# Kernel optimization log

Measured on AMD Instinct MI355X. Metric: run time of the kernel, lower is better.

## Reference

```python
import jax, jax.numpy as jnp
import numpy as np

# dims
B, T, H = 4, 2048, 768
HEADS, D = 4, 768          # GATConv(out_channels=768, heads=4, concat=False)
L = 3                      # num_layers
WIN = 2
K = 2 * WIN + 1
EPS = 1e-5
NEG_SLOPE = 0.2            # PyG GATConv leaky_relu slope


def setup_inputs() -> dict:
    key = jax.random.key(0)
    ks = jax.random.split(key, 4)
    s = 1.0 / np.sqrt(H)
    x = jax.random.normal(ks[0], (B, T, H), jnp.float32)
    W = jax.random.normal(ks[1], (L, H, HEADS, D), jnp.float32) * s   # lin weights per layer
    a_src = jax.random.normal(ks[2], (L, HEADS, D), jnp.float32) * s  # att_src
    a_dst = jax.random.normal(ks[3], (L, HEADS, D), jnp.float32) * s  # att_dst
    bias = jnp.zeros((L, D), jnp.float32)                             # GATConv bias (concat=False -> [D])
    gamma = jnp.ones((L, H), jnp.float32)                             # LayerNorm weight
    beta = jnp.zeros((L, H), jnp.float32)                             # LayerNorm bias
    return {"x": x, "W": W, "a_src": a_src, "a_dst": a_dst,
            "bias": bias, "gamma": gamma, "beta": beta}


def _layernorm(z, g, b):
    m = jnp.mean(z, axis=-1, keepdims=True)
    v = jnp.mean((z - m) ** 2, axis=-1, keepdims=True)
    return (z - m) * jax.lax.rsqrt(v + EPS) * g + b


def _gat_layer(x, Wl, asrc_w, adst_w, bias_l, idx, mask):
    # x: [B,T,H]; banded GAT with neighborhoods idx: [T,K] (clipped), mask: [T,K]
    h = jnp.einsum('bti,ihd->bthd', x, Wl)                 # [B,T,heads,D]
    asrc = jnp.einsum('bthd,hd->bth', h, asrc_w)           # per-source-node score term
    adst = jnp.einsum('bthd,hd->bth', h, adst_w)           # per-target-node score term
    h_nb = h[:, idx]                                       # [B,T,K,heads,D] gathered neighbors j
    score = jax.nn.leaky_relu(asrc[:, idx] + adst[:, :, None, :], NEG_SLOPE)  # [B,T,K,heads]
    score = jnp.where(mask[None, :, :, None], score, -jnp.inf)
    attn = jax.nn.softmax(score, axis=2)                   # softmax over incoming edges per target
    out = jnp.einsum('btkh,btkhd->bthd', attn, h_nb)       # weighted aggregation
    return out.mean(axis=2) + bias_l                       # concat=False -> mean over heads


def reference(x, W, a_src, a_dst, bias, gamma, beta):
    # banded neighborhood indices (window edges both directions + self-loop from PyG default)
    offs = jnp.arange(-WIN, WIN + 1)
    idx = jnp.arange(T)[:, None] + offs[None, :]           # [T,K]
    mask = (idx >= 0) & (idx < T)
    idx = jnp.clip(idx, 0, T - 1)
    for l in range(L):
        res = x
        y = _gat_layer(x, W[l], a_src[l], a_dst[l], bias[l], idx, mask)
        x = _layernorm(y + res, gamma[l], beta[l])         # dropout = identity in eval
    return x
```

## Files before the change

### kernel.cpp

```cpp
#include <hip/hip_runtime.h>
#include <stdint.h>

#define TT 2048
#define BB 4
#define HH 768
#define NHEADS 4
#define DD 768
#define NN 3072
#define LL 3
#define BT 8192
#define KNB 5
#define NBLK 12
#define ATPB 4
#define NROWS 8

typedef __bf16 bf16x8 __attribute__((ext_vector_type(8)));
typedef float f32x4 __attribute__((ext_vector_type(4)));

__device__ __forceinline__ unsigned short f2bf(float f){
  union { float f; unsigned u; } v; v.f = f;
  unsigned u = v.u;
  return (unsigned short)((u + 0x7FFFu + ((u >> 16) & 1u)) >> 16);
}
__device__ __forceinline__ float bf2f(unsigned short h){
  union { unsigned u; float f; } v; v.u = ((unsigned)h) << 16;
  return v.f;
}
__device__ __forceinline__ void gload16(const unsigned short* g, unsigned short* l){
  __builtin_amdgcn_global_load_lds((const __attribute__((address_space(1))) void*)g,
                                   (__attribute__((address_space(3))) void*)l, 16, 0, 0);
}

__global__ void wt_kernel(const float* __restrict__ W, unsigned short* __restrict__ Wt){
  __shared__ float tile[32][33];
  int l = blockIdx.z;
  int n0 = blockIdx.x * 32, k0 = blockIdx.y * 32;
  int tx = threadIdx.x, ty = threadIdx.y;
  const float* Wl = W + (size_t)l * HH * NN;
  for (int r = 0; r < 4; r++)
    tile[ty + r*8][tx] = Wl[(size_t)(k0 + ty + r*8) * NN + n0 + tx];
  __syncthreads();
  unsigned short* Wtl = Wt + (size_t)l * NN * HH;
  for (int r = 0; r < 4; r++){
    int n = n0 + ty + r*8;
    Wtl[(size_t)n * HH + k0 + tx] = f2bf(tile[tx][ty + r*8]);
  }
}

__global__ void xconv_kernel(const float* __restrict__ x, unsigned short* __restrict__ xb){
  int i = blockIdx.x * blockDim.x + threadIdx.x;
  float4 v = ((const float4*)x)[i];
  ushort4 o;
  o.x = f2bf(v.x); o.y = f2bf(v.y); o.z = f2bf(v.z); o.w = f2bf(v.w);
  *(ushort4*)(xb + (size_t)i * 4) = o;
}

#define BM 128
#define BN 128
#define BK 64

__global__ __launch_bounds__(256, 2) void gemm_kernel(
    const unsigned short* __restrict__ xb,
    const unsigned short* __restrict__ wt,
    unsigned short* __restrict__ hout,
    const float* __restrict__ a_srcl,
    const float* __restrict__ a_dstl,
    float* __restrict__ psrc,
    float* __restrict__ pdst){
  __shared__ __align__(16) unsigned short xs[BM][BK];
  __shared__ __align__(16) unsigned short wsd[BN][BK];
  int bm = blockIdx.y * BM;
  int bn = blockIdx.x * BN;
  int tid = threadIdx.x;
  int wave = tid >> 6, lane = tid & 63;
  int m16 = lane & 15, q = lane >> 4;
  int wm = (wave >> 1) * 64, wn = (wave & 1) * 64;
  int r8 = lane >> 3, c8 = lane & 7;
  int cg = (c8 ^ r8) * 8;
  const unsigned short* ga[4]; const unsigned short* gb[4];
  unsigned short* la[4]; unsigned short* lb[4];
  #pragma unroll
  for (int s = 0; s < 4; s++){
    int row = wave * 32 + s * 8;
    ga[s] = xb + (size_t)(bm + row + r8) * HH + cg;
    gb[s] = wt + (size_t)(bn + row + r8) * HH + cg;
    la[s] = &xs[row][0];
    lb[s] = &wsd[row][0];
  }
  int rd0 = ((0 + q) ^ (m16 & 7)) * 8;
  int rd1 = ((4 + q) ^ (m16 & 7)) * 8;
  f32x4 acc[4][4] = {};
  for (int k0 = 0; k0 < HH; k0 += BK){
    #pragma unroll
    for (int s = 0; s < 4; s++){
      gload16(ga[s] + k0, la[s]);
      gload16(gb[s] + k0, lb[s]);
    }
    __syncthreads();
    bf16x8 af[4], bfr[4];
    for (int i = 0; i < 4; i++)
      af[i] = __builtin_bit_cast(bf16x8, *(const uint4*)(&xs[wm + i*16 + m16][rd0]));
    for (int j = 0; j < 4; j++)
      bfr[j] = __builtin_bit_cast(bf16x8, *(const uint4*)(&wsd[wn + j*16 + m16][rd0]));
    for (int i = 0; i < 4; i++)
      for (int j = 0; j < 4; j++)
        acc[i][j] = __builtin_amdgcn_mfma_f32_16x16x32_bf16(af[i], bfr[j], acc[i][j], 0, 0, 0);
    for (int i = 0; i < 4; i++)
      af[i] = __builtin_bit_cast(bf16x8, *(const uint4*)(&xs[wm + i*16 + m16][rd1]));
    for (int j = 0; j < 4; j++)
      bfr[j] = __builtin_bit_cast(bf16x8, *(const uint4*)(&wsd[wn + j*16 + m16][rd1]));
    for (int i = 0; i < 4; i++)
      for (int j = 0; j < 4; j++)
        acc[i][j] = __builtin_amdgcn_mfma_f32_16x16x32_bf16(af[i], bfr[j], acc[i][j], 0, 0, 0);
    __syncthreads();
  }
  for (int i = 0; i < 4; i++){
    int row0 = bm + wm + i*16 + q*4;
    for (int j = 0; j < 4; j++){
      int col = bn + wn + j*16 + m16;
      unsigned short* hp = hout + (size_t)row0 * NN + col;
      hp[0]            = f2bf(acc[i][j][0]);
      hp[NN]           = f2bf(acc[i][j][1]);
      hp[2*(size_t)NN] = f2bf(acc[i][j][2]);
      hp[3*(size_t)NN] = f2bf(acc[i][j][3]);
    }
  }
  int col0 = bn + wn;
  int head = col0 / DD;
  int blk  = (col0 % DD) >> 6;
  float wsrc[4], wdstw[4];
  for (int j = 0; j < 4; j++){
    int n = col0 + j*16 + m16;
    wsrc[j]  = a_srcl[n];
    wdstw[j] = a_dstl[n];
  }
  for (int i = 0; i < 4; i++){
    for (int reg = 0; reg < 4; reg++){
      float ss = 0.f, dd = 0.f;
      for (int j = 0; j < 4; j++){
        float v = acc[i][j][reg];
        ss += v * wsrc[j];
        dd += v * wdstw[j];
      }
      ss += __shfl_xor(ss, 1, 64); dd += __shfl_xor(dd, 1, 64);
      ss += __shfl_xor(ss, 2, 64); dd += __shfl_xor(dd, 2, 64);
      ss += __shfl_xor(ss, 4, 64); dd += __shfl_xor(dd, 4, 64);
      ss += __shfl_xor(ss, 8, 64); dd += __shfl_xor(dd, 8, 64);
      if (m16 == 0){
        int row = bm + wm + i*16 + q*4 + reg;
        size_t slot = (size_t)row * (NHEADS * NBLK) + head * NBLK + blk;
        psrc[slot] = ss;
        pdst[slot] = dd;
      }
    }
  }
}

__global__ __launch_bounds__(384) void attn_ln_kernel(const unsigned short* __restrict__ h,
    const float* __restrict__ psrc, const float* __restrict__ pdst,
    const float* __restrict__ xin_f32,
    const unsigned short* __restrict__ xin_bf,
    const float* __restrict__ bias_l,
    const float* __restrict__ gamma_l, const float* __restrict__ beta_l,
    float* __restrict__ x_out, unsigned short* __restrict__ xb_next,
    int write_f32){
  int bid = blockIdx.x;
  int grp = ((bid & 7) << 8) | (bid >> 3);
  int token0 = grp * ATPB;
  int t0 = token0 & (TT - 1);
  int bseq = token0 >> 11;
  int tid = threadIdx.x;
  int wave = tid >> 6, lane = tid & 63;
  __shared__ __align__(16) unsigned short hs[NROWS][NN];
  __shared__ float attn_s[ATPB][NHEADS][KNB];
  __shared__ float as_sh[NROWS * NHEADS], ad_sh[NROWS * NHEADS];
  __shared__ float part_s[ATPB * 96], part_q[ATPB * 96];
  __shared__ float mv_mean[ATPB], mv_rstd[ATPB];
  #pragma unroll
  for (int j = 0; j < NROWS; j++){
    int g = t0 - 2 + j;
    g = min(max(g, 0), TT - 1);
    const unsigned short* src = h + ((size_t)(bseq * TT + g)) * NN + tid * 8;
    gload16(src, &hs[j][wave * 512]);
  }
  if (tid < 2 * NROWS * NHEADS){
    int which = tid >= NROWS * NHEADS;
    int i = tid & (NROWS * NHEADS - 1);
    int lt = i >> 2, head = i & 3;
    int tcl = min(max(t0 - 2 + lt, 0), TT - 1);
    const float* p = (which ? pdst : psrc) +
        ((size_t)(bseq * TT + tcl) * NHEADS + head) * NBLK;
    float4 a = *(const float4*)(p);
    float4 b = *(const float4*)(p + 4);
    float4 d = *(const float4*)(p + 8);
    float s = a.x+a.y+a.z+a.w + b.x+b.y+b.z+b.w + d.x+d.y+d.z+d.w;
    (which ? ad_sh : as_sh)[i] = s;
  }
  __syncthreads();
  if (tid < ATPB * NHEADS){
    int ti = tid >> 2, head = tid & 3;
    int t = t0 + ti;
    float sc[KNB];
    float mx = -3.0e38f;
    float ad = ad_sh[(ti + 2) * NHEADS + head];
    for (int k = 0; k < KNB; k++){
      int tn = t + k - 2;
      if (tn >= 0 && tn < TT){
        float s = as_sh[(ti + k) * NHEADS + head] + ad;
        s = s > 0.f ? s : 0.2f * s;
        sc[k] = s; mx = fmaxf(mx, s);
      } else sc[k] = -3.0e38f;
    }
    float den = 0.f;
    for (int k = 0; k < KNB; k++){
      float e = (sc[k] > -1.0e38f) ? __expf(sc[k] - mx) : 0.f;
      sc[k] = e; den += e;
    }
    float inv = 0.25f / den;
    for (int k = 0; k < KNB; k++) attn_s[ti][head][k] = sc[k] * inv;
  }
  __syncthreads();
  int ti = tid / 96, c = tid % 96;
  int token = token0 + ti;
  float ac[NHEADS][KNB];
  for (int hd = 0; hd < NHEADS; hd++)
    for (int k = 0; k < KNB; k++) ac[hd][k] = attn_s[ti][hd][k];
  float y8[8] = {};
  for (int hd = 0; hd < NHEADS; hd++){
    #pragma unroll
    for (int k = 0; k < KNB; k++){
      bf16x8 v = __builtin_bit_cast(bf16x8, *(const uint4*)(&hs[ti + k][hd * DD + c * 8]));
      float a = ac[hd][k];
      #pragma unroll
      for (int e = 0; e < 8; e++) y8[e] += a * (float)v[e];
    }
  }
  float xr[8], bb[8];
  if (xin_f32){
    const float4* p = (const float4*)&xin_f32[(size_t)token * HH + c * 8];
    *(float4*)&xr[0] = p[0]; *(float4*)&xr[4] = p[1];
  } else {
    uint4 u = *(const uint4*)&xin_bf[(size_t)token * HH + c * 8];
    const unsigned short* us = (const unsigned short*)&u;
    #pragma unroll
    for (int e = 0; e < 8; e++) xr[e] = bf2f(us[e]);
  }
  { const float4* p = (const float4*)&bias_l[c * 8];
    *(float4*)&bb[0] = p[0]; *(float4*)&bb[4] = p[1]; }
  float s = 0.f, sq = 0.f;
  #pragma unroll
  for (int e = 0; e < 8; e++){
    float zz = y8[e] + bb[e] + xr[e];
    y8[e] = zz; s += zz; sq += zz * zz;
  }
  part_s[tid] = s; part_q[tid] = sq;
  __syncthreads();
  if (wave < ATPB){
    float vs = part_s[wave * 96 + lane];
    float vq = part_q[wave * 96 + lane];
    if (lane < 32){
      vs += part_s[wave * 96 + 64 + lane];
      vq += part_q[wave * 96 + 64 + lane];
    }
    for (int off = 32; off > 0; off >>= 1){
      vs += __shfl_xor(vs, off, 64);
      vq += __shfl_xor(vq, off, 64);
    }
    if (lane == 0){
      float mean = vs * (1.f / HH);
      float var = vq * (1.f / HH) - mean * mean;
      mv_mean[wave] = mean;
      mv_rstd[wave] = rsqrtf(var + 1e-5f);
    }
  }
  __syncthreads();
  float mean = mv_mean[ti], rstd = mv_rstd[ti];
  float gr[8], br[8];
  { const float4* p = (const float4*)&gamma_l[c * 8];
    *(float4*)&gr[0] = p[0]; *(float4*)&gr[4] = p[1]; }
  { const float4* p = (const float4*)&beta_l[c * 8];
    *(float4*)&br[0] = p[0]; *(float4*)&br[4] = p[1]; }
  float o[8];
  #pragma unroll
  for (int e = 0; e < 8; e++)
    o[e] = (y8[e] - mean) * rstd * gr[e] + br[e];
  if (write_f32){
    float* xo = &x_out[(size_t)token * HH + c * 8];
    *(float4*)&xo[0] = *(float4*)&o[0];
    *(float4*)&xo[4] = *(float4*)&o[4];
  } else {
    unsigned short o16[8];
    #pragma unroll
    for (int e = 0; e < 8; e++) o16[e] = f2bf(o[e]);
    *(uint4*)(&xb_next[(size_t)token * HH + c * 8]) = *(uint4*)&o16[0];
  }
}

extern "C" void kernel_launch(void* const* d_in, const int* in_sizes, int n_in,
                              void* d_out, int out_size, void* d_ws, size_t ws_size,
                              hipStream_t stream) {
  const float* x     = (const float*)d_in[0];
  const float* W     = (const float*)d_in[1];
  const float* a_src = (const float*)d_in[2];
  const float* a_dst = (const float*)d_in[3];
  const float* bias  = (const float*)d_in[4];
  const float* gamma = (const float*)d_in[5];
  const float* beta  = (const float*)d_in[6];
  float* out = (float*)d_out;

  char* ws = (char*)d_ws;
  size_t off = 0;
  auto alloc = [&](size_t bytes)->char*{
    char* p = ws + off;
    off = (off + bytes + 255) & ~(size_t)255;
    return p;
  };
  unsigned short* wt   = (unsigned short*)alloc((size_t)LL * NN * HH * 2);
  unsigned short* xb   = (unsigned short*)alloc((size_t)BT * HH * 2);
  unsigned short* hbuf = (unsigned short*)alloc((size_t)BT * NN * 2);
  float* psrc  = (float*)alloc((size_t)BT * NHEADS * NBLK * 4);
  float* pdst  = (float*)alloc((size_t)BT * NHEADS * NBLK * 4);

  wt_kernel<<<dim3(NN/32, HH/32, LL), dim3(32, 8), 0, stream>>>(W, wt);
  xconv_kernel<<<(BT * HH / 4) / 256, 256, 0, stream>>>(x, xb);

  for (int l = 0; l < LL; l++){
    gemm_kernel<<<dim3(NN / BN, BT / BM), 256, 0, stream>>>(
        xb, wt + (size_t)l * NN * HH, hbuf,
        a_src + (size_t)l * NHEADS * DD, a_dst + (size_t)l * NHEADS * DD,
        psrc, pdst);
    attn_ln_kernel<<<BT / ATPB, 384, 0, stream>>>(hbuf, psrc, pdst,
        (l == 0) ? x : nullptr, xb,
        bias + (size_t)l * DD, gamma + (size_t)l * HH, beta + (size_t)l * HH,
        out, xb, (l == LL - 1) ? 1 : 0);
  }
}
```

Baseline: 340.5 us.

## Remap GEMM tiles per XCD, raise occupancy, and prefetch LN operands early

The GEMM grid becomes 1D and block IDs are remapped so that each XCD handles a contiguous slab of 8 M-tiles across all N-tiles. This aims to improve L2 reuse of the activation rows within each XCD. The launch bound now asks for 3 blocks per CU, which may cap registers and cause spills. The attention/LayerNorm kernel now issues its residual, bias, gamma and beta loads before the first barrier, overlapping their latency with the h-row staging.

New measurement: 335.2 us. No clear change (-1.6%).

```diff
diff --git a/kernel.cpp b/kernel.cpp
--- a/kernel.cpp
+++ b/kernel.cpp
@@ -59,7 +59,7 @@
 #define BN 128
 #define BK 64
 
-__global__ __launch_bounds__(256, 2) void gemm_kernel(
+__global__ __launch_bounds__(256, 3) void gemm_kernel(
     const unsigned short* __restrict__ xb,
     const unsigned short* __restrict__ wt,
     unsigned short* __restrict__ hout,
@@ -69,8 +69,13 @@
     float* __restrict__ pdst){
   __shared__ __align__(16) unsigned short xs[BM][BK];
   __shared__ __align__(16) unsigned short wsd[BN][BK];
-  int bm = blockIdx.y * BM;
-  int bn = blockIdx.x * BN;
+  int id = blockIdx.x;
+  int xcd = id & 7;
+  int s = id >> 3;
+  int bn_i = s / 8;
+  int bm_i = (s & 7) + xcd * 8;
+  int bm = bm_i * BM;
+  int bn = bn_i * BN;
   int tid = threadIdx.x;
   int wave = tid >> 6, lane = tid & 63;
   int m16 = lane & 15, q = lane >> 4;
@@ -80,21 +85,21 @@
   const unsigned short* ga[4]; const unsigned short* gb[4];
   unsigned short* la[4]; unsigned short* lb[4];
   #pragma unroll
-  for (int s = 0; s < 4; s++){
-    int row = wave * 32 + s * 8;
-    ga[s] = xb + (size_t)(bm + row + r8) * HH + cg;
-    gb[s] = wt + (size_t)(bn + row + r8) * HH + cg;
-    la[s] = &xs[row][0];
-    lb[s] = &wsd[row][0];
+  for (int ss = 0; ss < 4; ss++){
+    int row = wave * 32 + ss * 8;
+    ga[ss] = xb + (size_t)(bm + row + r8) * HH + cg;
+    gb[ss] = wt + (size_t)(bn + row + r8) * HH + cg;
+    la[ss] = &xs[row][0];
+    lb[ss] = &wsd[row][0];
   }
   int rd0 = ((0 + q) ^ (m16 & 7)) * 8;
   int rd1 = ((4 + q) ^ (m16 & 7)) * 8;
   f32x4 acc[4][4] = {};
   for (int k0 = 0; k0 < HH; k0 += BK){
     #pragma unroll
-    for (int s = 0; s < 4; s++){
-      gload16(ga[s] + k0, la[s]);
-      gload16(gb[s] + k0, lb[s]);
+    for (int ss = 0; ss < 4; ss++){
+      gload16(ga[ss] + k0, la[ss]);
+      gload16(gb[ss] + k0, lb[ss]);
     }
     __syncthreads();
     bf16x8 af[4], bfr[4];
@@ -171,6 +176,8 @@
   int bseq = token0 >> 11;
   int tid = threadIdx.x;
   int wave = tid >> 6, lane = tid & 63;
+  int ti = tid / 96, c = tid % 96;
+  int token = token0 + ti;
   __shared__ __align__(16) unsigned short hs[NROWS][NN];
   __shared__ float attn_s[ATPB][NHEADS][KNB];
   __shared__ float as_sh[NROWS * NHEADS], ad_sh[NROWS * NHEADS];
@@ -183,6 +190,22 @@
     const unsigned short* src = h + ((size_t)(bseq * TT + g)) * NN + tid * 8;
     gload16(src, &hs[j][wave * 512]);
   }
+  float xr[8], bb[8], gr[8], br[8];
+  if (xin_f32){
+    const float4* p = (const float4*)&xin_f32[(size_t)token * HH + c * 8];
+    *(float4*)&xr[0] = p[0]; *(float4*)&xr[4] = p[1];
+  } else {
+    uint4 u = *(const uint4*)&xin_bf[(size_t)token * HH + c * 8];
+    const unsigned short* us = (const unsigned short*)&u;
+    #pragma unroll
+    for (int e = 0; e < 8; e++) xr[e] = bf2f(us[e]);
+  }
+  { const float4* p = (const float4*)&bias_l[c * 8];
+    *(float4*)&bb[0] = p[0]; *(float4*)&bb[4] = p[1]; }
+  { const float4* p = (const float4*)&gamma_l[c * 8];
+    *(float4*)&gr[0] = p[0]; *(float4*)&gr[4] = p[1]; }
+  { const float4* p = (const float4*)&beta_l[c * 8];
+    *(float4*)&br[0] = p[0]; *(float4*)&br[4] = p[1]; }
   if (tid < 2 * NROWS * NHEADS){
     int which = tid >= NROWS * NHEADS;
     int i = tid & (NROWS * NHEADS - 1);
@@ -198,15 +221,15 @@
   }
   __syncthreads();
   if (tid < ATPB * NHEADS){
-    int ti = tid >> 2, head = tid & 3;
-    int t = t0 + ti;
+    int tii = tid >> 2, head = tid & 3;
+    int t = t0 + tii;
     float sc[KNB];
     float mx = -3.0e38f;
-    float ad = ad_sh[(ti + 2) * NHEADS + head];
+    float ad = ad_sh[(tii + 2) * NHEADS + head];
     for (int k = 0; k < KNB; k++){
       int tn = t + k - 2;
       if (tn >= 0 && tn < TT){
-        float s = as_sh[(ti + k) * NHEADS + head] + ad;
+        float s = as_sh[(tii + k) * NHEADS + head] + ad;
         s = s > 0.f ? s : 0.2f * s;
         sc[k] = s; mx = fmaxf(mx, s);
       } else sc[k] = -3.0e38f;
@@ -217,11 +240,9 @@
       sc[k] = e; den += e;
     }
     float inv = 0.25f / den;
-    for (int k = 0; k < KNB; k++) attn_s[ti][head][k] = sc[k] * inv;
-  }
-  __syncthreads();
-  int ti = tid / 96, c = tid % 96;
-  int token = token0 + ti;
+    for (int k = 0; k < KNB; k++) attn_s[tii][head][k] = sc[k] * inv;
+  }
+  __syncthreads();
   float ac[NHEADS][KNB];
   for (int hd = 0; hd < NHEADS; hd++)
     for (int k = 0; k < KNB; k++) ac[hd][k] = attn_s[ti][hd][k];
@@ -235,18 +256,6 @@
       for (int e = 0; e < 8; e++) y8[e] += a * (float)v[e];
     }
   }
-  float xr[8], bb[8];
-  if (xin_f32){
-    const float4* p = (const float4*)&xin_f32[(size_t)token * HH + c * 8];
-    *(float4*)&xr[0] = p[0]; *(float4*)&xr[4] = p[1];
-  } else {
-    uint4 u = *(const uint4*)&xin_bf[(size_t)token * HH + c * 8];
-    const unsigned short* us = (const unsigned short*)&u;
-    #pragma unroll
-    for (int e = 0; e < 8; e++) xr[e] = bf2f(us[e]);
-  }
-  { const float4* p = (const float4*)&bias_l[c * 8];
-    *(float4*)&bb[0] = p[0]; *(float4*)&bb[4] = p[1]; }
   float s = 0.f, sq = 0.f;
   #pragma unroll
   for (int e = 0; e < 8; e++){
@@ -275,11 +284,6 @@
   }
   __syncthreads();
   float mean = mv_mean[ti], rstd = mv_rstd[ti];
-  float gr[8], br[8];
-  { const float4* p = (const float4*)&gamma_l[c * 8];
-    *(float4*)&gr[0] = p[0]; *(float4*)&gr[4] = p[1]; }
-  { const float4* p = (const float4*)&beta_l[c * 8];
-    *(float4*)&br[0] = p[0]; *(float4*)&br[4] = p[1]; }
   float o[8];
   #pragma unroll
   for (int e = 0; e < 8; e++)
@@ -325,7 +329,7 @@
   xconv_kernel<<<(BT * HH / 4) / 256, 256, 0, stream>>>(x, xb);
 
   for (int l = 0; l < LL; l++){
-    gemm_kernel<<<dim3(NN / BN, BT / BM), 256, 0, stream>>>(
+    gemm_kernel<<<(NN / BN) * (BT / BM), 256, 0, stream>>>(
         xb, wt + (size_t)l * NN * HH, hbuf,
         a_src + (size_t)l * NHEADS * DD, a_dst + (size_t)l * NHEADS * DD,
         psrc, pdst);
```
